# Kernel tuning notes

Measured on AMD Instinct MI355X. Metric: run time of the kernel, lower is better.

Reference implementation:

```python
import jax, jax.numpy as jnp
import numpy as np

# node types: 0=atac_region 1=gene 2=tad 3=protein 4=protein_name 5=enhancer
N = [25000, 15000, 4000, 12000, 12000, 15000]
FEAT = [257, 129, 128, 128, 129, 128]
# 19 relations of the HeteroConv, as (src_type, dst_type)
REL = [(2,0),(0,2),(2,1),(1,2),(0,1),(1,0),(3,3),(3,1),(1,3),(3,1),(1,3),(3,4),(4,3),(5,0),(0,5),(5,1),(1,5),(0,1),(1,0)]
E = 100000
H, HID = 128, 256
NAMES = ['atac','gene','tad','protein','pname','enh']


def setup_inputs():
    rng = np.random.default_rng(0)
    w = lambda *s: jnp.asarray((rng.standard_normal(s) / np.sqrt(s[-2])).astype(np.float32))
    z = lambda *s: jnp.zeros(s, dtype=jnp.float32)
    inp = {}
    for L in (0, 1):
        for t, nm in enumerate(NAMES):
            inp[f"x_{nm}{L}"] = jnp.asarray(rng.standard_normal((N[t], FEAT[t])).astype(np.float32))
            # sorted unique global node ids (x_map)
            inp[f"map_{nm}{L}"] = jnp.asarray(np.sort(rng.choice(2 * N[t], size=N[t], replace=False)).astype(np.int32))
        e = np.empty((len(REL), 2, E), dtype=np.int32)
        for r, (s, d) in enumerate(REL):
            e[r, 0] = rng.integers(0, N[s], E)
            e[r, 1] = rng.integers(0, N[d], E)
        inp[f"edges{L}"] = jnp.asarray(e)
    inp.update(W_in_atac=w(257, H), b_in_atac=z(H), W_in_gene=w(129, H), b_in_gene=z(H), W_in_pname=w(129, H), b_in_pname=z(H))
    inp.update(conv_wl=w(19, H, H), conv_bl=z(19, H), conv_wr=w(19, H, H))
    inp.update(mlp_w1=w(6, H, HID), mlp_b1=z(6, HID), mlp_w2=w(6, HID, H), mlp_b2=z(6, H))
    inp.update(gd_w1=w(H, HID), gd_b1=z(HID), gd_w2=w(HID, 1), gd_b2=z(1),
               gv_w1=w(H, HID), gv_b1=z(HID), gv_w2=w(HID, 1), gv_b2=z(1))
    return inp


def _sage(x_src, x_dst, eidx, wl, bl, wr):
    # PyG SAGEConv: out = lin_l(mean_{j in N(i)} x_src[j]) + lin_r(x_dst[i])
    src, dst = eidx[0], eidx[1]
    nd = x_dst.shape[0]
    agg = jax.ops.segment_sum(x_src[src], dst, num_segments=nd)
    cnt = jax.ops.segment_sum(jnp.ones((src.shape[0],), x_src.dtype), dst, num_segments=nd)
    mean = agg / jnp.maximum(cnt, 1.0)[:, None]
    return mean @ wl + bl + x_dst @ wr


def _hetero(xs, edges, wl, bl, wr):
    # HeteroConv with default sum aggregation across relations sharing a dst type
    out = {}
    for r, (s, d) in enumerate(REL):
        o = _sage(xs[s], xs[d], edges[r], wl[r], bl[r], wr[r])
        out[d] = out[d] + o if d in out else o
    return out


def _forward(fl, maps0, maps1, edges0, edges1):
    (x_atac0, x_gene0, x_tad0, x_protein0, x_pname0, x_enh0,
     x_atac1, x_gene1, x_tad1, x_protein1, x_pname1, x_enh1,
     W_in_atac, b_in_atac, W_in_gene, b_in_gene, W_in_pname, b_in_pname,
     conv_wl, conv_bl, conv_wr,
     mlp_w1, mlp_b1, mlp_w2, mlp_b2,
     gd_w1, gd_b1, gd_w2, gd_b2, gv_w1, gv_b1, gv_w2, gv_b2) = fl
    # input_linear applied to protein_name / atac_region / gene of every layer snapshot
    xs0 = [x_atac0 @ W_in_atac + b_in_atac, x_gene0 @ W_in_gene + b_in_gene, x_tad0,
           x_protein0, x_pname0 @ W_in_pname + b_in_pname, x_enh0]
    xs1 = [x_atac1 @ W_in_atac + b_in_atac, x_gene1 @ W_in_gene + b_in_gene, x_tad1,
           x_protein1, x_pname1 @ W_in_pname + b_in_pname, x_enh1]
    # layer 0 hetero conv + per-node-type layer MLP
    new0 = _hetero(xs0, edges0, conv_wl, conv_bl, conv_wr)
    new0 = {d: jax.nn.relu(x @ mlp_w1[d] + mlp_b1[d]) @ mlp_w2[d] + mlp_b2[d] for d, x in new0.items()}
    # mask-based cross-layer scatter: next_layer.x[dst_mask] = new_x[src_mask]
    # (x_maps sorted & unique -> equivalent gather via argmax of the O(N^2) equality mask)
    for d, x in new0.items():
        Mm = maps0[d][:, None] == maps1[d][None, :]   # [N0_d, N1_d] bool
        dst_mask = Mm.any(axis=0)                      # next-layer nodes present in layer 0
        pos = jnp.argmax(Mm, axis=0)                   # matching layer-0 row per next node
        xs1[d] = jnp.where(dst_mask[:, None], x[pos], xs1[d])
    # final layer: hetero conv only (no layer MLP, per encode())
    new1 = _hetero(xs1, edges1, conv_wl, conv_bl, conv_wr)
    g = new1[1]  # target = 'gene'
    p_drop = jax.nn.sigmoid(jax.nn.relu(g @ gd_w1 + gd_b1) @ gd_w2 + gd_b2)
    values = jax.nn.relu(g @ gv_w1 + gv_b1) @ gv_w2 + gv_b2
    return jnp.concatenate([p_drop, values], axis=-1)  # [N_gene, 2]


def reference(x_atac0, x_gene0, x_tad0, x_protein0, x_pname0, x_enh0,
              x_atac1, x_gene1, x_tad1, x_protein1, x_pname1, x_enh1,
              map_atac0, map_gene0, map_tad0, map_protein0, map_pname0, map_enh0,
              map_atac1, map_gene1, map_tad1, map_protein1, map_pname1, map_enh1,
              edges0, edges1,
              W_in_atac, b_in_atac, W_in_gene, b_in_gene, W_in_pname, b_in_pname,
              conv_wl, conv_bl, conv_wr,
              mlp_w1, mlp_b1, mlp_w2, mlp_b2,
              gd_w1, gd_b1, gd_w2, gd_b2, gv_w1, gv_b1, gv_w2, gv_b2):
    maps0 = [map_atac0, map_gene0, map_tad0, map_protein0, map_pname0, map_enh0]
    maps1 = [map_atac1, map_gene1, map_tad1, map_protein1, map_pname1, map_enh1]
    fl = (x_atac0, x_gene0, x_tad0, x_protein0, x_pname0, x_enh0,
          x_atac1, x_gene1, x_tad1, x_protein1, x_pname1, x_enh1,
          W_in_atac, b_in_atac, W_in_gene, b_in_gene, W_in_pname, b_in_pname,
          conv_wl, conv_bl, conv_wr,
          mlp_w1, mlp_b1, mlp_w2, mlp_b2,
          gd_w1, gd_b1, gd_w2, gd_b2, gv_w1, gv_b1, gv_w2, gv_b2)
    return _forward(fl, maps0, maps1, edges0, edges1)
```

## Files before the change

kernel.cpp:

```cpp
#include <hip/hip_runtime.h>
#include <math.h>

#define E_EDGES 100000

typedef unsigned short u16;
typedef unsigned int u32;

using bfrag = __attribute__((ext_vector_type(8))) short;
using ffrag = __attribute__((ext_vector_type(4))) float;

__device__ inline float bf2f(u32 u) { union { u32 i; float f; } c; c.i = u << 16; return c.f; }
__device__ inline u16 f2bf(float f) {
  union { u32 i; float f; } c; c.f = f;
  u32 u = c.i;
  return (u16)((u + 0x7FFFu + ((u >> 16) & 1u)) >> 16);
}

struct CsrArgs { int relid[24]; int lay[24]; int nd[24]; int rpoff[24];
                 int bkoff[24]; int bboff[24]; int nb[24]; };

struct AggAllArgs {
  const u16* xsrc[23];
  const int* rowptr[23];
  const int* esrc[23];
  u16* dst[23];
  int nd[23]; int pitch[23]; int koff[23]; int selfs[23];
};

struct WTStackArgs {
  int srcrel[23]; int grp[23]; long outoff[23]; int koff[23]; int pitch[23];
  int gnr[5]; int grel[5][6];
};

struct WTArgs { const float* W[15]; u16* out[15]; int K[15]; int N[15]; int Kpad[15]; };
struct PadArgs { const float* src[11]; u16* dst[11]; int K[11]; int Kpad8[11];
                 int total[11]; int aligned[11]; };
struct InLinBArgs { const u16* A[5]; const u16* WT[5]; const float* bias[5]; u16* C[5];
                    int M[5]; int Kpad[5]; };
struct BGemmArgs { const u16* A[5]; const u16* WT[5]; const float* bias[5]; u16* C[5];
                   const int* POS[5]; int M[5]; };
struct PosArgs { const int* m0[5]; const int* m1[5]; int* pos[5]; int n[5]; };
struct HeadArgs { const u16* WT[2]; const float* b1[2]; float* hid[2]; const float* A; int M; };
struct HeadRArgs { const float* hid[2]; const float* w2[2]; const float* b2[2]; float* out; int M; };

template <int AF32, int OF32, int RELU>
__global__ __launch_bounds__(256) void tgemm(const void* __restrict__ Av,
                                             const u16* __restrict__ WT,
                                             const float* __restrict__ bias,
                                             void* __restrict__ Cv,
                                             int M, int K, int Kpad, int N)
{
  __shared__ u16 sA[64 * 40];
  __shared__ u16 sB[128 * 40];
  const int tid = threadIdx.x;
  const int w = tid >> 6, lane = tid & 63;
  const int quad = lane >> 4, m = lane & 15;
  const int rowbase = blockIdx.x * 64;
  const int colbase = blockIdx.y * 128;
  const int sr = tid >> 2, sc = tid & 3;
  const int br = tid >> 1, bh = tid & 1;
  ffrag acc[8];
  #pragma unroll
  for (int i = 0; i < 8; i++) { acc[i][0] = 0.f; acc[i][1] = 0.f; acc[i][2] = 0.f; acc[i][3] = 0.f; }

  for (int kt = 0; kt < Kpad / 32; kt++) {
    int gr = rowbase + sr, gk = kt * 32 + sc * 8;
    uint4 st = make_uint4(0, 0, 0, 0);
    if (AF32) {
      const float* A = (const float*)Av;
      if (gr < M) {
        const float* row = A + (long)gr * K + gk;
        float v[8];
        #pragma unroll
        for (int i = 0; i < 8; i++) v[i] = (gk + i < K) ? row[i] : 0.f;
        st.x = (u32)f2bf(v[0]) | ((u32)f2bf(v[1]) << 16);
        st.y = (u32)f2bf(v[2]) | ((u32)f2bf(v[3]) << 16);
        st.z = (u32)f2bf(v[4]) | ((u32)f2bf(v[5]) << 16);
        st.w = (u32)f2bf(v[6]) | ((u32)f2bf(v[7]) << 16);
      }
    } else {
      const u16* A = (const u16*)Av;
      if (gr < M) st = *(const uint4*)(A + (long)gr * K + gk);
    }
    const u16* wrow = WT + (long)(colbase + br) * Kpad + kt * 32 + bh * 16;
    uint4 b0 = *(const uint4*)wrow;
    uint4 b1 = *(const uint4*)(wrow + 8);

    if (kt) __syncthreads();
    *(uint4*)&sA[sr * 40 + sc * 8] = st;
    *(uint4*)&sB[br * 40 + bh * 16] = b0;
    *(uint4*)&sB[br * 40 + bh * 16 + 8] = b1;
    __syncthreads();

    bfrag a = *(const bfrag*)&sA[(w * 16 + m) * 40 + quad * 8];
    #pragma unroll
    for (int ct = 0; ct < 8; ct++) {
      bfrag b = *(const bfrag*)&sB[(ct * 16 + m) * 40 + quad * 8];
      acc[ct] = __builtin_amdgcn_mfma_f32_16x16x32_bf16(a, b, acc[ct], 0, 0, 0);
    }
  }

  #pragma unroll
  for (int ct = 0; ct < 8; ct++) {
    int col = colbase + ct * 16 + m;
    float bv = bias ? bias[col] : 0.f;
    #pragma unroll
    for (int r = 0; r < 4; r++) {
      int row = rowbase + w * 16 + quad * 4 + r;
      if (row < M) {
        float v = acc[ct][r] + bv;
        if (RELU) v = fmaxf(v, 0.f);
        long off = (long)row * N + col;
        if (OF32) ((float*)Cv)[off] = v;
        else ((u16*)Cv)[off] = f2bf(v);
      }
    }
  }
}

__global__ __launch_bounds__(256) void tgemm_inb(InLinBArgs a)
{
  const int z = blockIdx.z;
  const int M = a.M[z], Kpad = a.Kpad[z];
  const int rowbase = blockIdx.x * 64;
  if (rowbase >= M) return;
  __shared__ u16 sA[64 * 40];
  __shared__ u16 sB[128 * 40];
  const int tid = threadIdx.x;
  const int w = tid >> 6, lane = tid & 63;
  const int quad = lane >> 4, m = lane & 15;
  const int sr = tid >> 2, sc = tid & 3;
  const int br = tid >> 1, bh = tid & 1;
  const u16* A = a.A[z];
  const u16* WT = a.WT[z];
  ffrag acc[8];
  #pragma unroll
  for (int i = 0; i < 8; i++) { acc[i][0] = 0.f; acc[i][1] = 0.f; acc[i][2] = 0.f; acc[i][3] = 0.f; }

  for (int kt = 0; kt < Kpad / 32; kt++) {
    int gr = rowbase + sr, gk = kt * 32 + sc * 8;
    uint4 st = make_uint4(0, 0, 0, 0);
    if (gr < M) st = *(const uint4*)(A + (long)gr * Kpad + gk);
    const u16* wrow = WT + (long)br * Kpad + kt * 32 + bh * 16;
    uint4 b0 = *(const uint4*)wrow;
    uint4 b1 = *(const uint4*)(wrow + 8);

    if (kt) __syncthreads();
    *(uint4*)&sA[sr * 40 + sc * 8] = st;
    *(uint4*)&sB[br * 40 + bh * 16] = b0;
    *(uint4*)&sB[br * 40 + bh * 16 + 8] = b1;
    __syncthreads();

    bfrag av = *(const bfrag*)&sA[(w * 16 + m) * 40 + quad * 8];
    #pragma unroll
    for (int ct = 0; ct < 8; ct++) {
      bfrag bv = *(const bfrag*)&sB[(ct * 16 + m) * 40 + quad * 8];
      acc[ct] = __builtin_amdgcn_mfma_f32_16x16x32_bf16(av, bv, acc[ct], 0, 0, 0);
    }
  }

  const float* bias = a.bias[z];
  u16* C = a.C[z];
  #pragma unroll
  for (int ct = 0; ct < 8; ct++) {
    int col = ct * 16 + m;
    float bv = bias[col];
    #pragma unroll
    for (int r = 0; r < 4; r++) {
      int row = rowbase + w * 16 + quad * 4 + r;
      if (row < M) C[(long)row * 128 + col] = f2bf(acc[ct][r] + bv);
    }
  }
}

__global__ __launch_bounds__(256) void tgemm_m1b(BGemmArgs a)
{
  const int z = blockIdx.z;
  const int M = a.M[z];
  const int rowbase = blockIdx.x * 64;
  if (rowbase >= M) return;
  const int colbase = blockIdx.y * 128;
  __shared__ u16 sA[64 * 40];
  __shared__ u16 sB[128 * 40];
  const int tid = threadIdx.x;
  const int w = tid >> 6, lane = tid & 63;
  const int quad = lane >> 4, m = lane & 15;
  const int sr = tid >> 2, sc = tid & 3;
  const int br = tid >> 1, bh = tid & 1;
  const u16* A = a.A[z];
  const u16* WT = a.WT[z];
  ffrag acc[8];
  #pragma unroll
  for (int i = 0; i < 8; i++) { acc[i][0] = 0.f; acc[i][1] = 0.f; acc[i][2] = 0.f; acc[i][3] = 0.f; }

  for (int kt = 0; kt < 4; kt++) {
    int gr = rowbase + sr, gk = kt * 32 + sc * 8;
    uint4 st = make_uint4(0, 0, 0, 0);
    if (gr < M) st = *(const uint4*)(A + (long)gr * 128 + gk);
    const u16* wrow = WT + (long)(colbase + br) * 128 + kt * 32 + bh * 16;
    uint4 b0 = *(const uint4*)wrow;
    uint4 b1 = *(const uint4*)(wrow + 8);

    if (kt) __syncthreads();
    *(uint4*)&sA[sr * 40 + sc * 8] = st;
    *(uint4*)&sB[br * 40 + bh * 16] = b0;
    *(uint4*)&sB[br * 40 + bh * 16 + 8] = b1;
    __syncthreads();

    bfrag av = *(const bfrag*)&sA[(w * 16 + m) * 40 + quad * 8];
    #pragma unroll
    for (int ct = 0; ct < 8; ct++) {
      bfrag bv = *(const bfrag*)&sB[(ct * 16 + m) * 40 + quad * 8];
      acc[ct] = __builtin_amdgcn_mfma_f32_16x16x32_bf16(av, bv, acc[ct], 0, 0, 0);
    }
  }

  const float* bias = a.bias[z];
  u16* C = a.C[z];
  #pragma unroll
  for (int ct = 0; ct < 8; ct++) {
    int col = colbase + ct * 16 + m;
    float bv = bias[col];
    #pragma unroll
    for (int r = 0; r < 4; r++) {
      int row = rowbase + w * 16 + quad * 4 + r;
      if (row < M) C[(long)row * 256 + col] = f2bf(fmaxf(acc[ct][r] + bv, 0.f));
    }
  }
}

__global__ __launch_bounds__(256) void tgemm_scatb(BGemmArgs a)
{
  const int z = blockIdx.z;
  const int M = a.M[z];
  const int rowbase = blockIdx.x * 64;
  if (rowbase >= M) return;
  __shared__ u16 sA[64 * 40];
  __shared__ u16 sB[128 * 40];
  const int tid = threadIdx.x;
  const int w = tid >> 6, lane = tid & 63;
  const int quad = lane >> 4, m = lane & 15;
  const int sr = tid >> 2, sc = tid & 3;
  const int br = tid >> 1, bh = tid & 1;
  const u16* A = a.A[z];
  const u16* WT = a.WT[z];
  ffrag acc[8];
  #pragma unroll
  for (int i = 0; i < 8; i++) { acc[i][0] = 0.f; acc[i][1] = 0.f; acc[i][2] = 0.f; acc[i][3] = 0.f; }

  for (int kt = 0; kt < 8; kt++) {
    int gr = rowbase + sr, gk = kt * 32 + sc * 8;
    uint4 st = make_uint4(0, 0, 0, 0);
    if (gr < M) st = *(const uint4*)(A + (long)gr * 256 + gk);
    const u16* wrow = WT + (long)br * 256 + kt * 32 + bh * 16;
    uint4 b0 = *(const uint4*)wrow;
    uint4 b1 = *(const uint4*)(wrow + 8);

    if (kt) __syncthreads();
    *(uint4*)&sA[sr * 40 + sc * 8] = st;
    *(uint4*)&sB[br * 40 + bh * 16] = b0;
    *(uint4*)&sB[br * 40 + bh * 16 + 8] = b1;
    __syncthreads();

    bfrag av = *(const bfrag*)&sA[(w * 16 + m) * 40 + quad * 8];
    #pragma unroll
    for (int ct = 0; ct < 8; ct++) {
      bfrag bv = *(const bfrag*)&sB[(ct * 16 + m) * 40 + quad * 8];
      acc[ct] = __builtin_amdgcn_mfma_f32_16x16x32_bf16(av, bv, acc[ct], 0, 0, 0);
    }
  }

  const int* POS = a.POS[z];
  const float* bias = a.bias[z];
  u16* C = a.C[z];
  #pragma unroll
  for (int ct = 0; ct < 8; ct++) {
    int col = ct * 16 + m;
    float bv = bias[col];
    #pragma unroll
    for (int r = 0; r < 4; r++) {
      int row = rowbase + w * 16 + quad * 4 + r;
      if (row < M) {
        int j = POS[row];
        if (j >= 0) C[(long)j * 128 + col] = f2bf(acc[ct][r] + bv);
      }
    }
  }
}

__global__ __launch_bounds__(256) void padcvt_kernel(PadArgs a)
{
  const int z = blockIdx.y;
  int idx = blockIdx.x * 256 + threadIdx.x;
  if (idx >= a.total[z]) return;
  const int kp8 = a.Kpad8[z];
  const int K = a.K[z];
  int row = idx / kp8;
  int c8 = idx - row * kp8;
  int base = c8 * 8;
  u32 wv[4];
  if (a.aligned[z]) {
    const float4* src = (const float4*)(a.src[z] + (long)row * K + base);
    float4 f0 = src[0];
    float4 f1 = src[1];
    wv[0] = (u32)f2bf(f0.x) | ((u32)f2bf(f0.y) << 16);
    wv[1] = (u32)f2bf(f0.z) | ((u32)f2bf(f0.w) << 16);
    wv[2] = (u32)f2bf(f1.x) | ((u32)f2bf(f1.y) << 16);
    wv[3] = (u32)f2bf(f1.z) | ((u32)f2bf(f1.w) << 16);
  } else {
    const float* src = a.src[z] + (long)row * K + base;
    #pragma unroll
    for (int i = 0; i < 4; i++) {
      float lo = (base + 2 * i     < K) ? src[2 * i]     : 0.f;
      float hi = (base + 2 * i + 1 < K) ? src[2 * i + 1] : 0.f;
      wv[i] = (u32)f2bf(lo) | ((u32)f2bf(hi) << 16);
    }
  }
  *(uint4*)(a.dst[z] + (long)row * (kp8 * 8) + base) = make_uint4(wv[0], wv[1], wv[2], wv[3]);
}

__global__ __launch_bounds__(256) void tgemm_head(HeadArgs a)
{
  const int z = blockIdx.z;
  const int M = a.M;
  const int rowbase = blockIdx.x * 64;
  const int colbase = blockIdx.y * 128;
  __shared__ u16 sA[64 * 40];
  __shared__ u16 sB[128 * 40];
  const int tid = threadIdx.x;
  const int w = tid >> 6, lane = tid & 63;
  const int quad = lane >> 4, m = lane & 15;
  const int sr = tid >> 2, sc = tid & 3;
  const int br = tid >> 1, bh = tid & 1;
  const float* A = a.A;
  const u16* WT = a.WT[z];
  ffrag acc[8];
  #pragma unroll
  for (int i = 0; i < 8; i++) { acc[i][0] = 0.f; acc[i][1] = 0.f; acc[i][2] = 0.f; acc[i][3] = 0.f; }

  for (int kt = 0; kt < 4; kt++) {
    int gr = rowbase + sr, gk = kt * 32 + sc * 8;
    uint4 st = make_uint4(0, 0, 0, 0);
    if (gr < M) {
      const float4* row = (const float4*)(A + (long)gr * 128 + gk);
      float4 f0 = row[0];
      float4 f1 = row[1];
      st.x = (u32)f2bf(f0.x) | ((u32)f2bf(f0.y) << 16);
      st.y = (u32)f2bf(f0.z) | ((u32)f2bf(f0.w) << 16);
      st.z = (u32)f2bf(f1.x) | ((u32)f2bf(f1.y) << 16);
      st.w = (u32)f2bf(f1.z) | ((u32)f2bf(f1.w) << 16);
    }
    const u16* wrow = WT + (long)(colbase + br) * 128 + kt * 32 + bh * 16;
    uint4 b0 = *(const uint4*)wrow;
    uint4 b1 = *(const uint4*)(wrow + 8);

    if (kt) __syncthreads();
    *(uint4*)&sA[sr * 40 + sc * 8] = st;
    *(uint4*)&sB[br * 40 + bh * 16] = b0;
    *(uint4*)&sB[br * 40 + bh * 16 + 8] = b1;
    __syncthreads();

    bfrag av = *(const bfrag*)&sA[(w * 16 + m) * 40 + quad * 8];
    #pragma unroll
    for (int ct = 0; ct < 8; ct++) {
      bfrag bv = *(const bfrag*)&sB[(ct * 16 + m) * 40 + quad * 8];
      acc[ct] = __builtin_amdgcn_mfma_f32_16x16x32_bf16(av, bv, acc[ct], 0, 0, 0);
    }
  }

  const float* bias = a.b1[z];
  float* C = a.hid[z];
  #pragma unroll
  for (int ct = 0; ct < 8; ct++) {
    int col = colbase + ct * 16 + m;
    float bv = bias[col];
    #pragma unroll
    for (int r = 0; r < 4; r++) {
      int row = rowbase + w * 16 + quad * 4 + r;
      if (row < M) C[(long)row * 256 + col] = fmaxf(acc[ct][r] + bv, 0.f);
    }
  }
}

__global__ __launch_bounds__(256) void bhist_kernel(const int* __restrict__ e0,
                                                    const int* __restrict__ e1,
                                                    int* __restrict__ bcnt, CsrArgs a)
{
  const int slot = blockIdx.x / 25;
  const int ch = blockIdx.x % 25;
  const int base = ch * 4096;
  const int n = (E_EDGES - base < 4096) ? (E_EDGES - base) : 4096;
  const int* E = a.lay[slot] ? e1 : e0;
  const int r = a.relid[slot];
  const int tid = threadIdx.x;
  __shared__ int h[256];
  h[tid] = 0;
  __syncthreads();
  const int* darr = E + (r * 2 + 1) * E_EDGES + base;
  for (int i = tid; i < n; i += 256) atomicAdd(&h[darr[i] >> 7], 1);
  __syncthreads();
  if (tid < a.nb[slot] && h[tid]) atomicAdd(&bcnt[a.bkoff[slot] + tid], h[tid]);
}

__global__ __launch_bounds__(256) void bscan_kernel(const int* __restrict__ bcnt,
// ... 130 lines not shown
  int sr = a.srcrel[slot];
  float v;
  if (sr >= 0) {
    v = wl[(long)sr * 16384 + krel * 128 + n];
  } else {
    int g = a.grp[slot];
    v = 0.f;
    for (int i = 0; i < a.gnr[g]; i++) v += wr[(long)a.grel[g][i] * 16384 + krel * 128 + n];
    if (t < 128) {
      float b = 0.f;
      for (int i = 0; i < a.gnr[g]; i++) b += bl[a.grel[g][i] * 128 + t];
      BLS[g * 128 + t] = b;
    }
  }
  WTG[a.outoff[slot] + (long)n * a.pitch[slot] + a.koff[slot] + krel] = f2bf(v);
}

__global__ __launch_bounds__(256) void wt_kernel(WTArgs a)
{
  int s = blockIdx.y;
  int idx = blockIdx.x * 256 + threadIdx.x;
  int K = a.K[s], N = a.N[s], Kpad = a.Kpad[s];
  if (idx >= N * Kpad) return;
  int n = idx / Kpad, k = idx - n * Kpad;
  a.out[s][idx] = (k < K) ? f2bf(a.W[s][(long)k * N + n]) : (u16)0;
}

__global__ __launch_bounds__(256) void pos_kernel(PosArgs a)
{
  int g = blockIdx.y;
  int i = blockIdx.x * 256 + threadIdx.x;
  if (i >= a.n[g]) return;
  int key = a.m0[g][i];
  const int* m1 = a.m1[g];
  int lo = 0, hi = a.n[g] - 1, pos = -1;
  while (lo <= hi) {
    int mid = (lo + hi) >> 1;
    int v = m1[mid];
    if (v == key) { pos = mid; break; }
    if (v < key) lo = mid + 1; else hi = mid - 1;
  }
  a.pos[g][i] = pos;
}

__global__ __launch_bounds__(256) void agg_all(AggAllArgs a)
{
  int slot = blockIdx.y;
  int grp = threadIdx.x >> 4;
  int lane = threadIdx.x & 15;
  int row = blockIdx.x * 16 + grp;
  if (row >= a.nd[slot]) return;
  u16* dst = a.dst[slot] + (long)row * a.pitch[slot] + a.koff[slot] + lane * 8;
  const uint4* x4 = (const uint4*)a.xsrc[slot];
  if (a.selfs[slot]) {
    *(uint4*)dst = x4[(long)row * 16 + lane];
    return;
  }
  const int* rp = a.rowptr[slot];
  int c0 = rp[row], c1 = rp[row + 1];
  const int* es = a.esrc[slot];
  float acc[8];
  #pragma unroll
  for (int i = 0; i < 8; i++) acc[i] = 0.f;
  int e = c0;
  for (; e + 4 <= c1; e += 4) {
    int s0 = es[e], s1 = es[e + 1], s2 = es[e + 2], s3 = es[e + 3];
    uint4 v0 = x4[(long)s0 * 16 + lane];
    uint4 v1 = x4[(long)s1 * 16 + lane];
    uint4 v2 = x4[(long)s2 * 16 + lane];
    uint4 v3 = x4[(long)s3 * 16 + lane];
    const u32* w0 = (const u32*)&v0;
    const u32* w1 = (const u32*)&v1;
    const u32* w2 = (const u32*)&v2;
    const u32* w3 = (const u32*)&v3;
    #pragma unroll
    for (int i = 0; i < 4; i++) {
      acc[2*i]   += bf2f(w0[i] & 0xFFFF) + bf2f(w1[i] & 0xFFFF)
                  + bf2f(w2[i] & 0xFFFF) + bf2f(w3[i] & 0xFFFF);
      acc[2*i+1] += bf2f(w0[i] >> 16) + bf2f(w1[i] >> 16)
                  + bf2f(w2[i] >> 16) + bf2f(w3[i] >> 16);
    }
  }
  for (; e < c1; e++) {
    uint4 v = x4[(long)es[e] * 16 + lane];
    const u32* wv = (const u32*)&v;
    #pragma unroll
    for (int i = 0; i < 4; i++) {
      acc[2*i]   += bf2f(wv[i] & 0xFFFF);
      acc[2*i+1] += bf2f(wv[i] >> 16);
    }
  }
  int c = c1 - c0;
  float inv = 1.f / (float)(c > 1 ? c : 1);
  u32 o[4];
  #pragma unroll
  for (int i = 0; i < 4; i++)
    o[i] = (u32)f2bf(acc[2*i] * inv) | ((u32)f2bf(acc[2*i+1] * inv) << 16);
  *(uint4*)dst = make_uint4(o[0], o[1], o[2], o[3]);
}

__global__ __launch_bounds__(256) void head_reduce2(HeadRArgs a)
{
  int wave = threadIdx.x >> 6, lane = threadIdx.x & 63;
  int row = blockIdx.x * 4 + wave;
  int z = blockIdx.y;
  if (row >= a.M) return;
  const float* h = a.hid[z] + (long)row * 256;
  const float* w2 = a.w2[z];
  float s = h[lane] * w2[lane] + h[lane + 64] * w2[lane + 64]
          + h[lane + 128] * w2[lane + 128] + h[lane + 192] * w2[lane + 192];
  #pragma unroll
  for (int off = 32; off >= 1; off >>= 1) s += __shfl_down(s, off, 64);
  if (lane == 0) {
    float v = s + a.b2[z][0];
    if (z == 0) v = 1.0f / (1.0f + expf(-v));
    a.out[row * 2 + z] = v;
  }
}

extern "C" void kernel_launch(void* const* d_in, const int* in_sizes, int n_in,
                              void* d_out, int out_size, void* d_ws, size_t ws_size,
                              hipStream_t stream)
{
  static const int NT[6] = {25000, 15000, 4000, 12000, 12000, 15000};
  static const int REL_S[19] = {2,0,2,1,0,1,3,3,1,3,1,3,4,5,0,5,1,0,1};
  static const int REL_D[19] = {0,2,1,2,1,0,3,1,3,1,3,4,3,0,5,1,5,1,0};

  auto xin   = [&](int t, int L) { return (const float*)d_in[L * 13 + 2 * t]; };
  auto mapin = [&](int t, int L) { return (const int*)d_in[L * 13 + 2 * t + 1]; };
  const int* edges0 = (const int*)d_in[12];
  const int* edges1 = (const int*)d_in[25];
  const float* W_in_atac  = (const float*)d_in[26];
  const float* b_in_atac  = (const float*)d_in[27];
  const float* W_in_gene  = (const float*)d_in[28];
  const float* b_in_gene  = (const float*)d_in[29];
  const float* W_in_pname = (const float*)d_in[30];
  const float* b_in_pname = (const float*)d_in[31];
  const float* conv_wl = (const float*)d_in[32];
  const float* conv_bl = (const float*)d_in[33];
  const float* conv_wr = (const float*)d_in[34];
  const float* mlp_w1 = (const float*)d_in[35];
  const float* mlp_b1 = (const float*)d_in[36];
  const float* mlp_w2 = (const float*)d_in[37];
  const float* mlp_b2 = (const float*)d_in[38];
  const float* gd_w1 = (const float*)d_in[39];
  const float* gd_b1 = (const float*)d_in[40];
  const float* gd_w2 = (const float*)d_in[41];
  const float* gd_b2 = (const float*)d_in[42];
  const float* gv_w1 = (const float*)d_in[43];
  const float* gv_b1 = (const float*)d_in[44];
  const float* gv_w2 = (const float*)d_in[45];
  const float* gv_b2 = (const float*)d_in[46];
  float* out = (float*)d_out;

  static const int GD[5]       = {0, 1, 2, 3, 5};
  static const int GNR[5]      = {4, 6, 2, 4, 2};
  static const int GRELS[5][6] = {{0,5,13,18,0,0},{2,4,7,9,15,17},{1,3,0,0,0,0},
                                  {6,8,10,12,0,0},{14,16,0,0,0,0}};
  static const int GPITCH[5]   = {640, 896, 384, 640, 384};

  float* fp = (float*)d_ws;
  auto takef = [&](size_t n) { float* q = fp; fp += n; return q; };
  float* BLS  = takef(5 * 128);
  float* G1   = takef((size_t)15000 * 128);
  u16* bp = (u16*)fp;
  auto takeb = [&](size_t n) { u16* q = bp; bp += n; return q; };
  u16* XB0[6]; u16* XB1[6];
  XB0[0] = takeb((size_t)25000 * 128);
  XB0[1] = takeb((size_t)15000 * 128);
  XB0[2] = takeb((size_t)4000 * 128);
  XB0[3] = takeb((size_t)12000 * 128);
  XB0[4] = takeb((size_t)12000 * 128);
  XB0[5] = takeb((size_t)15000 * 128);
  XB1[0] = takeb((size_t)25000 * 128);
  XB1[1] = takeb((size_t)15000 * 128);
  XB1[2] = takeb((size_t)4000 * 128);
  XB1[3] = takeb((size_t)12000 * 128);
  XB1[4] = nullptr;
  XB1[5] = takeb((size_t)15000 * 128);
  u16* ABUF = takeb((size_t)44416000);
  u16* ABUFg[5];
  {
    long o = 0;
    for (int g = 0; g < 5; g++) { ABUFg[g] = ABUF + o; o += (long)NT[GD[g]] * GPITCH[g]; }
  }
  u16* NWB  = takeb((size_t)71000 * 128);
  u16* HIDB = takeb((size_t)71000 * 256);
  u16* NWBg[5]; u16* HIDBg[5];
  {
    long o = 0;
    for (int g = 0; g < 5; g++) { NWBg[g] = NWB + o * 128; HIDBg[g] = HIDB + o * 256; o += NT[GD[g]]; }
  }
  u16* WTG  = takeb(376832);
  u16* WTIA = takeb(128 * 288);
  u16* WTIG = takeb(128 * 160);
  u16* WTIP = takeb(128 * 160);
  u16* WTM1 = takeb((size_t)5 * 32768);
  u16* WTM2 = takeb((size_t)5 * 32768);
  u16* WTHD = takeb(32768);
  u16* WTHV = takeb(32768);
  uintptr_t ipa = ((uintptr_t)bp + 15) & ~(uintptr_t)15;
  int* ip = (int*)ipa;
  auto takei = [&](size_t n) { int* q = ip; ip += n; return q; };
  int* RP    = takei(366024);
  int* BCNT  = takei(4704);
  int* BBASE = takei(4728);
  int* BCUR  = takei(4704);
  int* POSB  = takei(71000);
  int* ESRC  = takei((size_t)24 * E_EDGES);
  u32* TMP = (u32*)ABUF;
  float* HIDF0 = (float*)ABUF;
  float* HIDF1 = (float*)(ABUF + (size_t)15000 * 256 * 2);
  u16* PAD[5];
  PAD[0] = ABUF;
  PAD[1] = ABUF +  7200000;
  PAD[2] = ABUF +  9600000;
  PAD[3] = ABUF + 11520000;
  PAD[4] = ABUF + 18720000;

  long gbaseT[5];
  {
    long o = 0;
    for (int g = 0; g < 5; g++) { gbaseT[g] = o; o += (long)128 * GPITCH[g]; }
  }
  int* POSg[5];
  {
    int o = 0;
    for (int g = 0; g < 5; g++) { POSg[g] = POSB + o; o += NT[GD[g]]; }
  }

  {
    WTStackArgs wa{};
    int j = 0;
    for (int g = 0; g < 5; g++) {
      wa.gnr[g] = GNR[g];
      for (int i = 0; i < 6; i++) wa.grel[g][i] = GRELS[g][i];
      for (int s = 0; s <= GNR[g]; s++, j++) {
        wa.srcrel[j] = (s < GNR[g]) ? GRELS[g][s] : -1;
        wa.grp[j] = g;
        wa.outoff[j] = gbaseT[g];
        wa.koff[j] = s * 128;
        wa.pitch[j] = GPITCH[g];
      }
    }
    hipLaunchKernelGGL(wtstack_kernel, dim3(64, 23), dim3(256), 0, stream,
// ... 50 lines not shown
    auto add = [&](int s, const u16* A, const u16* WT, const float* b, u16* C,
                   int M, int Kpad) {
      ia.A[s] = A; ia.WT[s] = WT; ia.bias[s] = b; ia.C[s] = C;
      ia.M[s] = M; ia.Kpad[s] = Kpad;
    };
    add(0, PAD[0], WTIA, b_in_atac,  XB0[0], 25000, 288);
    add(1, PAD[1], WTIG, b_in_gene,  XB0[1], 15000, 160);
    add(2, PAD[2], WTIP, b_in_pname, XB0[4], 12000, 160);
    add(3, PAD[3], WTIA, b_in_atac,  XB1[0], 25000, 288);
    add(4, PAD[4], WTIG, b_in_gene,  XB1[1], 15000, 160);
    hipLaunchKernelGGL(tgemm_inb, dim3(391, 1, 5), dim3(256), 0, stream, ia);
  }

  static const int L0R[18] = {0,1,2,3,4,5,6,7,8,9,10,12,13,14,15,16,17,18};
  static const int L1R[6]  = {2, 4, 7, 9, 15, 17};
  int rpoffByRel[19], slotByRel[19], rpoff1[19], slot1[19];
  CsrArgs cc{};
  {
    int ro = 0, bo = 0, s = 0;
    for (int i = 0; i < 18; i++, s++) {
      int r = L0R[i];
      cc.relid[s] = r; cc.lay[s] = 0; int nd = NT[REL_D[r]];
      cc.nd[s] = nd; cc.rpoff[s] = ro;
      cc.bkoff[s] = bo; cc.bboff[s] = bo + s; cc.nb[s] = (nd + 127) >> 7;
      rpoffByRel[r] = ro; slotByRel[r] = s;
      ro += nd + 1; bo += cc.nb[s];
    }
    for (int i = 0; i < 6; i++, s++) {
      int r = L1R[i];
      cc.relid[s] = r; cc.lay[s] = 1;
      cc.nd[s] = 15000; cc.rpoff[s] = ro;
      cc.bkoff[s] = bo; cc.bboff[s] = bo + s; cc.nb[s] = (15000 + 127) >> 7;
      rpoff1[r] = ro; slot1[r] = s;
      ro += 15001; bo += cc.nb[s];
    }
    hipMemsetAsync(BCNT, 0, (size_t)bo * 4, stream);
    hipLaunchKernelGGL(bhist_kernel, dim3(24 * 25), dim3(256), 0, stream, edges0, edges1, BCNT, cc);
    hipLaunchKernelGGL(bscan_kernel, dim3(24), dim3(256), 0, stream, BCNT, BBASE, BCUR, cc);
    hipLaunchKernelGGL(bucket_scatter, dim3(24 * 25), dim3(256), 0, stream,
                       edges0, edges1, BCUR, TMP, cc);
    hipLaunchKernelGGL(bucket_to_csr, dim3(196, 24), dim3(256), 0, stream, TMP, BBASE, RP, ESRC, cc);
  }

  {
    AggAllArgs aa{};
    int j = 0;
    for (int g = 0; g < 5; g++) {
      int d = GD[g];
      for (int i = 0; i < GNR[g]; i++, j++) {
        int r = GRELS[g][i];
        aa.xsrc[j]   = XB0[REL_S[r]];
        aa.rowptr[j] = RP + rpoffByRel[r];
        aa.esrc[j]   = ESRC + (long)slotByRel[r] * E_EDGES;
        aa.dst[j] = ABUFg[g]; aa.nd[j] = NT[d]; aa.pitch[j] = GPITCH[g];
        aa.koff[j] = i * 128; aa.selfs[j] = 0;
      }
      aa.xsrc[j] = XB0[d]; aa.rowptr[j] = nullptr; aa.esrc[j] = nullptr;
      aa.dst[j] = ABUFg[g]; aa.nd[j] = NT[d]; aa.pitch[j] = GPITCH[g];
      aa.koff[j] = GNR[g] * 128; aa.selfs[j] = 1; j++;
    }
    hipLaunchKernelGGL(agg_all, dim3(1563, 23), dim3(256), 0, stream, aa);
  }
  {
    InLinBArgs ia{};
    for (int g = 0; g < 5; g++) {
      ia.A[g] = ABUFg[g]; ia.WT[g] = WTG + gbaseT[g]; ia.bias[g] = BLS + g * 128;
      ia.C[g] = NWBg[g]; ia.M[g] = NT[GD[g]]; ia.Kpad[g] = GPITCH[g];
    }
    hipLaunchKernelGGL(tgemm_inb, dim3(391, 1, 5), dim3(256), 0, stream, ia);
  }
  {
    BGemmArgs ba{};
    for (int g = 0; g < 5; g++) {
      int d = GD[g];
      ba.A[g] = NWBg[g]; ba.WT[g] = WTM1 + (long)g * 32768; ba.bias[g] = mlp_b1 + d * 256;
      ba.C[g] = HIDBg[g]; ba.POS[g] = nullptr; ba.M[g] = NT[d];
    }
    hipLaunchKernelGGL(tgemm_m1b, dim3(391, 2, 5), dim3(256), 0, stream, ba);
  }
  {
    BGemmArgs ba{};
    for (int g = 0; g < 5; g++) {
      int d = GD[g];
      ba.A[g] = HIDBg[g]; ba.WT[g] = WTM2 + (long)g * 32768; ba.bias[g] = mlp_b2 + d * 128;
      ba.C[g] = XB1[d]; ba.POS[g] = POSg[g]; ba.M[g] = NT[d];
    }
    hipLaunchKernelGGL(tgemm_scatb, dim3(391, 1, 5), dim3(256), 0, stream, ba);
  }

  {
    AggAllArgs aa{};
    for (int i = 0; i < 6; i++) {
      int r = L1R[i];
      aa.xsrc[i]   = XB1[REL_S[r]];
      aa.rowptr[i] = RP + rpoff1[r];
      aa.esrc[i]   = ESRC + (long)slot1[r] * E_EDGES;
      aa.dst[i] = ABUF; aa.nd[i] = 15000; aa.pitch[i] = 896;
      aa.koff[i] = i * 128; aa.selfs[i] = 0;
    }
    aa.xsrc[6] = XB1[1]; aa.rowptr[6] = nullptr; aa.esrc[6] = nullptr;
    aa.dst[6] = ABUF; aa.nd[6] = 15000; aa.pitch[6] = 896;
    aa.koff[6] = 6 * 128; aa.selfs[6] = 1;
    hipLaunchKernelGGL(agg_all, dim3(938, 7), dim3(256), 0, stream, aa);
    hipLaunchKernelGGL(HIP_KERNEL_NAME(tgemm<0,1,0>), dim3(235, 1), dim3(256), 0, stream,
                       (const void*)ABUF, WTG + gbaseT[1], BLS + 1 * 128, (void*)G1,
                       15000, 896, 896, 128);
  }

  {
    HeadArgs ha{};
    ha.WT[0] = WTHD; ha.WT[1] = WTHV;
    ha.b1[0] = gd_b1; ha.b1[1] = gv_b1;
    ha.hid[0] = HIDF0; ha.hid[1] = HIDF1;
    ha.A = G1; ha.M = 15000;
    hipLaunchKernelGGL(tgemm_head, dim3(235, 2, 2), dim3(256), 0, stream, ha);
    HeadRArgs hr{};
    hr.hid[0] = HIDF0; hr.hid[1] = HIDF1;
    hr.w2[0] = gd_w2; hr.w2[1] = gv_w2;
    hr.b2[0] = gd_b2; hr.b2[1] = gv_b2;
    hr.out = out; hr.M = 15000;
    hipLaunchKernelGGL(head_reduce2, dim3(3750, 2), dim3(256), 0, stream, hr);
  }
}
```

Baseline: 547.2 us.

## Fuse conv linear and two-layer MLP into one kernel, drop self-copy slots

Layer-0 conv projection, MLP hidden layer and MLP output with position scatter now run in one fused kernel that keeps the intermediate 64-row tiles in LDS instead of writing them to global buffers between three launches. The aggregation kernel no longer copies self features into the concatenated buffer; the GEMMs read self features straight from the node feature array by splitting the K range. The layer-1 conv output is stored as bf16 rather than fp32, and the head kernel reads it without converting. In exchange, the larger LDS footprint (about 50KB) lowers occupancy, and the fused kernel serializes its three GEMM phases within each block.

```diff
diff --git a/kernel.cpp b/kernel.cpp
--- a/kernel.cpp
+++ b/kernel.cpp
@@ -20,11 +20,11 @@
                  int bkoff[24]; int bboff[24]; int nb[24]; };
 
 struct AggAllArgs {
-  const u16* xsrc[23];
-  const int* rowptr[23];
-  const int* esrc[23];
-  u16* dst[23];
-  int nd[23]; int pitch[23]; int koff[23]; int selfs[23];
+  const u16* xsrc[18];
+  const int* rowptr[18];
+  const int* esrc[18];
+  u16* dst[18];
+  int nd[18]; int pitch[18]; int koff[18];
 };
 
 struct WTStackArgs {
@@ -37,86 +37,14 @@
                  int total[11]; int aligned[11]; };
 struct InLinBArgs { const u16* A[5]; const u16* WT[5]; const float* bias[5]; u16* C[5];
                     int M[5]; int Kpad[5]; };
-struct BGemmArgs { const u16* A[5]; const u16* WT[5]; const float* bias[5]; u16* C[5];
-                   const int* POS[5]; int M[5]; };
+struct FusedArgs {
+  const u16* A[5]; const u16* selfA[5]; const u16* WTC[5]; const float* biasC[5];
+  const u16* W1[5]; const float* b1[5]; const u16* W2[5]; const float* b2[5];
+  const int* POS[5]; u16* C[5]; int M[5]; int kself[5]; int Kpad[5];
+};
 struct PosArgs { const int* m0[5]; const int* m1[5]; int* pos[5]; int n[5]; };
-struct HeadArgs { const u16* WT[2]; const float* b1[2]; float* hid[2]; const float* A; int M; };
+struct HeadArgs { const u16* WT[2]; const float* b1[2]; float* hid[2]; const u16* A; int M; };
 struct HeadRArgs { const float* hid[2]; const float* w2[2]; const float* b2[2]; float* out; int M; };
-
-template <int AF32, int OF32, int RELU>
-__global__ __launch_bounds__(256) void tgemm(const void* __restrict__ Av,
-                                             const u16* __restrict__ WT,
-                                             const float* __restrict__ bias,
-                                             void* __restrict__ Cv,
-                                             int M, int K, int Kpad, int N)
-{
-  __shared__ u16 sA[64 * 40];
-  __shared__ u16 sB[128 * 40];
-  const int tid = threadIdx.x;
-  const int w = tid >> 6, lane = tid & 63;
-  const int quad = lane >> 4, m = lane & 15;
-  const int rowbase = blockIdx.x * 64;
-  const int colbase = blockIdx.y * 128;
-  const int sr = tid >> 2, sc = tid & 3;
-  const int br = tid >> 1, bh = tid & 1;
-  ffrag acc[8];
-  #pragma unroll
-  for (int i = 0; i < 8; i++) { acc[i][0] = 0.f; acc[i][1] = 0.f; acc[i][2] = 0.f; acc[i][3] = 0.f; }
-
-  for (int kt = 0; kt < Kpad / 32; kt++) {
-    int gr = rowbase + sr, gk = kt * 32 + sc * 8;
-    uint4 st = make_uint4(0, 0, 0, 0);
-    if (AF32) {
-      const float* A = (const float*)Av;
-      if (gr < M) {
-        const float* row = A + (long)gr * K + gk;
-        float v[8];
-        #pragma unroll
-        for (int i = 0; i < 8; i++) v[i] = (gk + i < K) ? row[i] : 0.f;
-        st.x = (u32)f2bf(v[0]) | ((u32)f2bf(v[1]) << 16);
-        st.y = (u32)f2bf(v[2]) | ((u32)f2bf(v[3]) << 16);
-        st.z = (u32)f2bf(v[4]) | ((u32)f2bf(v[5]) << 16);
-        st.w = (u32)f2bf(v[6]) | ((u32)f2bf(v[7]) << 16);
-      }
-    } else {
-      const u16* A = (const u16*)Av;
-      if (gr < M) st = *(const uint4*)(A + (long)gr * K + gk);
-    }
-    const u16* wrow = WT + (long)(colbase + br) * Kpad + kt * 32 + bh * 16;
-    uint4 b0 = *(const uint4*)wrow;
-    uint4 b1 = *(const uint4*)(wrow + 8);
-
-    if (kt) __syncthreads();
-    *(uint4*)&sA[sr * 40 + sc * 8] = st;
-    *(uint4*)&sB[br * 40 + bh * 16] = b0;
-    *(uint4*)&sB[br * 40 + bh * 16 + 8] = b1;
-    __syncthreads();
-
-    bfrag a = *(const bfrag*)&sA[(w * 16 + m) * 40 + quad * 8];
-    #pragma unroll
-    for (int ct = 0; ct < 8; ct++) {
-      bfrag b = *(const bfrag*)&sB[(ct * 16 + m) * 40 + quad * 8];
-      acc[ct] = __builtin_amdgcn_mfma_f32_16x16x32_bf16(a, b, acc[ct], 0, 0, 0);
-    }
-  }
-
-  #pragma unroll
-  for (int ct = 0; ct < 8; ct++) {
-    int col = colbase + ct * 16 + m;
-    float bv = bias ? bias[col] : 0.f;
-    #pragma unroll
-    for (int r = 0; r < 4; r++) {
-      int row = rowbase + w * 16 + quad * 4 + r;
-      if (row < M) {
-        float v = acc[ct][r] + bv;
-        if (RELU) v = fmaxf(v, 0.f);
-        long off = (long)row * N + col;
-        if (OF32) ((float*)Cv)[off] = v;
-        else ((u16*)Cv)[off] = f2bf(v);
-      }
-    }
-  }
-}
 
 __global__ __launch_bounds__(256) void tgemm_inb(InLinBArgs a)
 {
@@ -173,66 +101,154 @@
   }
 }
 
-__global__ __launch_bounds__(256) void tgemm_m1b(BGemmArgs a)
+__global__ __launch_bounds__(256) void fused_mlp(FusedArgs a)
 {
   const int z = blockIdx.z;
   const int M = a.M[z];
   const int rowbase = blockIdx.x * 64;
   if (rowbase >= M) return;
-  const int colbase = blockIdx.y * 128;
-  __shared__ u16 sA[64 * 40];
-  __shared__ u16 sB[128 * 40];
+  __shared__ u16 LDS[25088];
+  u16* sB  = LDS;
+  u16* sA  = LDS + 5120;
+  u16* m1  = LDS + 7680;
+  u16* m2b = LDS + 5120;
+  u16* m2a = LDS + 16384;
   const int tid = threadIdx.x;
   const int w = tid >> 6, lane = tid & 63;
   const int quad = lane >> 4, m = lane & 15;
   const int sr = tid >> 2, sc = tid & 3;
   const int br = tid >> 1, bh = tid & 1;
+  const int kself = a.kself[z], Kpad = a.Kpad[z];
   const u16* A = a.A[z];
-  const u16* WT = a.WT[z];
-  ffrag acc[8];
-  #pragma unroll
-  for (int i = 0; i < 8; i++) { acc[i][0] = 0.f; acc[i][1] = 0.f; acc[i][2] = 0.f; acc[i][3] = 0.f; }
-
-  for (int kt = 0; kt < 4; kt++) {
-    int gr = rowbase + sr, gk = kt * 32 + sc * 8;
-    uint4 st = make_uint4(0, 0, 0, 0);
-    if (gr < M) st = *(const uint4*)(A + (long)gr * 128 + gk);
-    const u16* wrow = WT + (long)(colbase + br) * 128 + kt * 32 + bh * 16;
-    uint4 b0 = *(const uint4*)wrow;
-    uint4 b1 = *(const uint4*)(wrow + 8);
-
-    if (kt) __syncthreads();
-    *(uint4*)&sA[sr * 40 + sc * 8] = st;
-    *(uint4*)&sB[br * 40 + bh * 16] = b0;
-    *(uint4*)&sB[br * 40 + bh * 16 + 8] = b1;
-    __syncthreads();
-
-    bfrag av = *(const bfrag*)&sA[(w * 16 + m) * 40 + quad * 8];
+  const u16* selfA = a.selfA[z];
+
+  {
+    const u16* WT = a.WTC[z];
+    ffrag acc[8];
+    #pragma unroll
+    for (int i = 0; i < 8; i++) { acc[i][0] = 0.f; acc[i][1] = 0.f; acc[i][2] = 0.f; acc[i][3] = 0.f; }
+    for (int kt = 0; kt < Kpad / 32; kt++) {
+      int gr = rowbase + sr, gk = kt * 32 + sc * 8;
+      uint4 st = make_uint4(0, 0, 0, 0);
+      if (gr < M) {
+        const u16* src = (gk < kself) ? (A + (long)gr * kself + gk)
+                                      : (selfA + (long)gr * 128 + (gk - kself));
+        st = *(const uint4*)src;
+      }
+      const u16* wrow = WT + (long)br * Kpad + kt * 32 + bh * 16;
+      uint4 b0 = *(const uint4*)wrow;
+      uint4 b1 = *(const uint4*)(wrow + 8);
+
+      if (kt) __syncthreads();
+      *(uint4*)&sA[sr * 40 + sc * 8] = st;
+      *(uint4*)&sB[br * 40 + bh * 16] = b0;
+      *(uint4*)&sB[br * 40 + bh * 16 + 8] = b1;
+      __syncthreads();
+
+      bfrag av = *(const bfrag*)&sA[(w * 16 + m) * 40 + quad * 8];
+      #pragma unroll
+      for (int ct = 0; ct < 8; ct++) {
+        bfrag bv = *(const bfrag*)&sB[(ct * 16 + m) * 40 + quad * 8];
+        acc[ct] = __builtin_amdgcn_mfma_f32_16x16x32_bf16(av, bv, acc[ct], 0, 0, 0);
+      }
+    }
+    const float* bc = a.biasC[z];
     #pragma unroll
     for (int ct = 0; ct < 8; ct++) {
-      bfrag bv = *(const bfrag*)&sB[(ct * 16 + m) * 40 + quad * 8];
-      acc[ct] = __builtin_amdgcn_mfma_f32_16x16x32_bf16(av, bv, acc[ct], 0, 0, 0);
-    }
-  }
-
-  const float* bias = a.bias[z];
-  u16* C = a.C[z];
-  #pragma unroll
-  for (int ct = 0; ct < 8; ct++) {
-    int col = colbase + ct * 16 + m;
-    float bv = bias[col];
-    #pragma unroll
-    for (int r = 0; r < 4; r++) {
-      int row = rowbase + w * 16 + quad * 4 + r;
-      if (row < M) C[(long)row * 256 + col] = f2bf(fmaxf(acc[ct][r] + bv, 0.f));
-    }
-  }
-}
-
-__global__ __launch_bounds__(256) void tgemm_scatb(BGemmArgs a)
-{
-  const int z = blockIdx.z;
-  const int M = a.M[z];
+      int col = ct * 16 + m;
+      float bv = bc[col];
+      #pragma unroll
+      for (int r = 0; r < 4; r++) {
+        int row = w * 16 + quad * 4 + r;
+        m1[row * 136 + col] = f2bf(acc[ct][r] + bv);
+      }
+    }
+  }
+
+  {
+    const u16* W1 = a.W1[z];
+    const float* b1p = a.b1[z];
+    for (int h = 0; h < 2; h++) {
+      ffrag acch[8];
+      #pragma unroll
+      for (int i = 0; i < 8; i++) { acch[i][0] = 0.f; acch[i][1] = 0.f; acch[i][2] = 0.f; acch[i][3] = 0.f; }
+      for (int kt = 0; kt < 4; kt++) {
+        const u16* wrow = W1 + (long)(h * 128 + br) * 128 + kt * 32 + bh * 16;
+        uint4 b0 = *(const uint4*)wrow;
+        uint4 b1v = *(const uint4*)(wrow + 8);
+        __syncthreads();
+        *(uint4*)&sB[br * 40 + bh * 16] = b0;
+        *(uint4*)&sB[br * 40 + bh * 16 + 8] = b1v;
+        __syncthreads();
+        bfrag av = *(const bfrag*)&m1[(w * 16 + m) * 136 + kt * 32 + quad * 8];
+        #pragma unroll
+        for (int ct = 0; ct < 8; ct++) {
+          bfrag bv = *(const bfrag*)&sB[(ct * 16 + m) * 40 + quad * 8];
+          acch[ct] = __builtin_amdgcn_mfma_f32_16x16x32_bf16(av, bv, acch[ct], 0, 0, 0);
+        }
+      }
+      u16* dstm = h ? m2b : m2a;
+      if (h) __syncthreads();
+      #pragma unroll
+      for (int ct = 0; ct < 8; ct++) {
+        int col = ct * 16 + m;
+        float bv = b1p[h * 128 + col];
+        #pragma unroll
+        for (int r = 0; r < 4; r++) {
+          int row = w * 16 + quad * 4 + r;
+          dstm[row * 136 + col] = f2bf(fmaxf(acch[ct][r] + bv, 0.f));
+        }
+      }
+    }
+  }
+
+  {
+    const u16* W2 = a.W2[z];
+    ffrag acc2[8];
+    #pragma unroll
+    for (int i = 0; i < 8; i++) { acc2[i][0] = 0.f; acc2[i][1] = 0.f; acc2[i][2] = 0.f; acc2[i][3] = 0.f; }
+    for (int kt = 0; kt < 8; kt++) {
+      const u16* wrow = W2 + (long)br * 256 + kt * 32 + bh * 16;
+      uint4 b0 = *(const uint4*)wrow;
+      uint4 b1v = *(const uint4*)(wrow + 8);
+      __syncthreads();
+      *(uint4*)&sB[br * 40 + bh * 16] = b0;
+      *(uint4*)&sB[br * 40 + bh * 16 + 8] = b1v;
+      __syncthreads();
+      const u16* msrc = (kt < 4) ? m2a : m2b;
+      bfrag av = *(const bfrag*)&msrc[(w * 16 + m) * 136 + (kt & 3) * 32 + quad * 8];
+      #pragma unroll
+      for (int ct = 0; ct < 8; ct++) {
+        bfrag bv = *(const bfrag*)&sB[(ct * 16 + m) * 40 + quad * 8];
+        acc2[ct] = __builtin_amdgcn_mfma_f32_16x16x32_bf16(av, bv, acc2[ct], 0, 0, 0);
+      }
+    }
+    const int* POS = a.POS[z];
+    const float* b2p = a.b2[z];
+    u16* C = a.C[z];
+    #pragma unroll
+    for (int ct = 0; ct < 8; ct++) {
+      int col = ct * 16 + m;
+      float bv = b2p[col];
+      #pragma unroll
+      for (int r = 0; r < 4; r++) {
+        int row = rowbase + w * 16 + quad * 4 + r;
+        if (row < M) {
+          int j = POS[row];
+          if (j >= 0) C[(long)j * 128 + col] = f2bf(acc2[ct][r] + bv);
+        }
+      }
+    }
+  }
+}
+
+__global__ __launch_bounds__(256) void conv_l1(const u16* __restrict__ A,
+                                               const u16* __restrict__ selfA,
+                                               const u16* __restrict__ WT,
+                                               const float* __restrict__ bias,
+                                               u16* __restrict__ C,
+                                               int M, int kself, int Kpad)
+{
   const int rowbase = blockIdx.x * 64;
   if (rowbase >= M) return;
   __shared__ u16 sA[64 * 40];
@@ -242,17 +258,19 @@
   const int quad = lane >> 4, m = lane & 15;
   const int sr = tid >> 2, sc = tid & 3;
   const int br = tid >> 1, bh = tid & 1;
-  const u16* A = a.A[z];
-  const u16* WT = a.WT[z];
   ffrag acc[8];
   #pragma unroll
   for (int i = 0; i < 8; i++) { acc[i][0] = 0.f; acc[i][1] = 0.f; acc[i][2] = 0.f; acc[i][3] = 0.f; }
 
-  for (int kt = 0; kt < 8; kt++) {
+  for (int kt = 0; kt < Kpad / 32; kt++) {
     int gr = rowbase + sr, gk = kt * 32 + sc * 8;
     uint4 st = make_uint4(0, 0, 0, 0);
-    if (gr < M) st = *(const uint4*)(A + (long)gr * 256 + gk);
-    const u16* wrow = WT + (long)br * 256 + kt * 32 + bh * 16;
+    if (gr < M) {
+      const u16* src = (gk < kself) ? (A + (long)gr * kself + gk)
+                                    : (selfA + (long)gr * 128 + (gk - kself));
+      st = *(const uint4*)src;
+    }
+    const u16* wrow = WT + (long)br * Kpad + kt * 32 + bh * 16;
     uint4 b0 = *(const uint4*)wrow;
     uint4 b1 = *(const uint4*)(wrow + 8);
 
@@ -270,9 +288,6 @@
     }
   }
 
-  const int* POS = a.POS[z];
-  const float* bias = a.bias[z];
-  u16* C = a.C[z];
   #pragma unroll
   for (int ct = 0; ct < 8; ct++) {
     int col = ct * 16 + m;
@@ -280,10 +295,7 @@
     #pragma unroll
     for (int r = 0; r < 4; r++) {
       int row = rowbase + w * 16 + quad * 4 + r;
-      if (row < M) {
-        int j = POS[row];
-        if (j >= 0) C[(long)j * 128 + col] = f2bf(acc[ct][r] + bv);
-      }
+      if (row < M) C[(long)row * 128 + col] = f2bf(acc[ct][r] + bv);
     }
   }
 }
@@ -332,7 +344,7 @@
   const int quad = lane >> 4, m = lane & 15;
   const int sr = tid >> 2, sc = tid & 3;
   const int br = tid >> 1, bh = tid & 1;
-  const float* A = a.A;
+  const u16* A = a.A;
   const u16* WT = a.WT[z];
   ffrag acc[8];
   #pragma unroll
@@ -341,15 +353,7 @@
   for (int kt = 0; kt < 4; kt++) {
     int gr = rowbase + sr, gk = kt * 32 + sc * 8;
     uint4 st = make_uint4(0, 0, 0, 0);
-    if (gr < M) {
-      const float4* row = (const float4*)(A + (long)gr * 128 + gk);
-      float4 f0 = row[0];
-      float4 f1 = row[1];
-      st.x = (u32)f2bf(f0.x) | ((u32)f2bf(f0.y) << 16);
-      st.y = (u32)f2bf(f0.z) | ((u32)f2bf(f0.w) << 16);
-      st.z = (u32)f2bf(f1.x) | ((u32)f2bf(f1.y) << 16);
-      st.w = (u32)f2bf(f1.z) | ((u32)f2bf(f1.w) << 16);
-    }
+    if (gr < M) st = *(const uint4*)(A + (long)gr * 128 + gk);
     const u16* wrow = WT + (long)(colbase + br) * 128 + kt * 32 + bh * 16;
     uint4 b0 = *(const uint4*)wrow;
     uint4 b1 = *(const uint4*)(wrow + 8);
@@ -586,10 +590,6 @@
   if (row >= a.nd[slot]) return;
   u16* dst = a.dst[slot] + (long)row * a.pitch[slot] + a.koff[slot] + lane * 8;
   const uint4* x4 = (const uint4*)a.xsrc[slot];
-  if (a.selfs[slot]) {
-    *(uint4*)dst = x4[(long)row * 16 + lane];
-    return;
-  }
   const int* rp = a.rowptr[slot];
   int c0 = rp[row], c1 = rp[row + 1];
   const int* es = a.esrc[slot];
@@ -692,11 +692,11 @@
   static const int GRELS[5][6] = {{0,5,13,18,0,0},{2,4,7,9,15,17},{1,3,0,0,0,0},
                                   {6,8,10,12,0,0},{14,16,0,0,0,0}};
   static const int GPITCH[5]   = {640, 896, 384, 640, 384};
+  static const int GPA[5]      = {512, 768, 256, 512, 256};
 
   float* fp = (float*)d_ws;
   auto takef = [&](size_t n) { float* q = fp; fp += n; return q; };
   float* BLS  = takef(5 * 128);
-  float* G1   = takef((size_t)15000 * 128);
   u16* bp = (u16*)fp;
   auto takeb = [&](size_t n) { u16* q = bp; bp += n; return q; };
   u16* XB0[6]; u16* XB1[6];
@@ -712,19 +712,13 @@
   XB1[3] = takeb((size_t)12000 * 128);
   XB1[4] = nullptr;
   XB1[5] = takeb((size_t)15000 * 128);
-  u16* ABUF = takeb((size_t)44416000);
+  u16* ABUF = takeb((size_t)35328000);
   u16* ABUFg[5];
   {
     long o = 0;
-    for (int g = 0; g < 5; g++) { ABUFg[g] = ABUF + o; o += (long)NT[GD[g]] * GPITCH[g]; }
-  }
-  u16* NWB  = takeb((size_t)71000 * 128);
-  u16* HIDB = takeb((size_t)71000 * 256);
-  u16* NWBg[5]; u16* HIDBg[5];
-  {
-    long o = 0;
-    for (int g = 0; g < 5; g++) { NWBg[g] = NWB + o * 128; HIDBg[g] = HIDB + o * 256; o += NT[GD[g]]; }
-  }
+    for (int g = 0; g < 5; g++) { ABUFg[g] = ABUF + o; o += (long)NT[GD[g]] * GPA[g]; }
+  }
+  u16* G1B  = takeb((size_t)15000 * 128);
   u16* WTG  = takeb(376832);
   u16* WTIA = takeb(128 * 288);
   u16* WTIG = takeb(128 * 160);
@@ -881,40 +875,24 @@
         aa.xsrc[j]   = XB0[REL_S[r]];
         aa.rowptr[j] = RP + rpoffByRel[r];
         aa.esrc[j]   = ESRC + (long)slotByRel[r] * E_EDGES;
-        aa.dst[j] = ABUFg[g]; aa.nd[j] = NT[d]; aa.pitch[j] = GPITCH[g];
-        aa.koff[j] = i * 128; aa.selfs[j] = 0;
+        aa.dst[j] = ABUFg[g]; aa.nd[j] = NT[d]; aa.pitch[j] = GPA[g];
+        aa.koff[j] = i * 128;
       }
-      aa.xsrc[j] = XB0[d]; aa.rowptr[j] = nullptr; aa.esrc[j] = nullptr;
-      aa.dst[j] = ABUFg[g]; aa.nd[j] = NT[d]; aa.pitch[j] = GPITCH[g];
-      aa.koff[j] = GNR[g] * 128; aa.selfs[j] = 1; j++;
-    }
-    hipLaunchKernelGGL(agg_all, dim3(1563, 23), dim3(256), 0, stream, aa);
-  }
-  {
-    InLinBArgs ia{};
-    for (int g = 0; g < 5; g++) {
-      ia.A[g] = ABUFg[g]; ia.WT[g] = WTG + gbaseT[g]; ia.bias[g] = BLS + g * 128;
-      ia.C[g] = NWBg[g]; ia.M[g] = NT[GD[g]]; ia.Kpad[g] = GPITCH[g];
-    }
-    hipLaunchKernelGGL(tgemm_inb, dim3(391, 1, 5), dim3(256), 0, stream, ia);
-  }
-  {
-    BGemmArgs ba{};
+    }
+    hipLaunchKernelGGL(agg_all, dim3(1563, 18), dim3(256), 0, stream, aa);
+  }
+  {
+    FusedArgs fa{};
     for (int g = 0; g < 5; g++) {
       int d = GD[g];
-      ba.A[g] = NWBg[g]; ba.WT[g] = WTM1 + (long)g * 32768; ba.bias[g] = mlp_b1 + d * 256;
-      ba.C[g] = HIDBg[g]; ba.POS[g] = nullptr; ba.M[g] = NT[d];
-    }
-    hipLaunchKernelGGL(tgemm_m1b, dim3(391, 2, 5), dim3(256), 0, stream, ba);
-  }
-  {
-    BGemmArgs ba{};
-    for (int g = 0; g < 5; g++) {
-      int d = GD[g];
-      ba.A[g] = HIDBg[g]; ba.WT[g] = WTM2 + (long)g * 32768; ba.bias[g] = mlp_b2 + d * 128;
-      ba.C[g] = XB1[d]; ba.POS[g] = POSg[g]; ba.M[g] = NT[d];
-    }
-    hipLaunchKernelGGL(tgemm_scatb, dim3(391, 1, 5), dim3(256), 0, stream, ba);
+      fa.A[g] = ABUFg[g]; fa.selfA[g] = XB0[d];
+      fa.WTC[g] = WTG + gbaseT[g]; fa.biasC[g] = BLS + g * 128;
+      fa.W1[g] = WTM1 + (long)g * 32768; fa.b1[g] = mlp_b1 + d * 256;
+      fa.W2[g] = WTM2 + (long)g * 32768; fa.b2[g] = mlp_b2 + d * 128;
+      fa.POS[g] = POSg[g]; fa.C[g] = XB1[d];
+      fa.M[g] = NT[d]; fa.kself[g] = GPA[g]; fa.Kpad[g] = GPITCH[g];
+    }
+    hipLaunchKernelGGL(fused_mlp, dim3(391, 1, 5), dim3(256), 0, stream, fa);
   }
 
   {
@@ -924,16 +902,13 @@
       aa.xsrc[i]   = XB1[REL_S[r]];
       aa.rowptr[i] = RP + rpoff1[r];
       aa.esrc[i]   = ESRC + (long)slot1[r] * E_EDGES;
-      aa.dst[i] = ABUF; aa.nd[i] = 15000; aa.pitch[i] = 896;
-      aa.koff[i] = i * 128; aa.selfs[i] = 0;
-    }
-    aa.xsrc[6] = XB1[1]; aa.rowptr[6] = nullptr; aa.esrc[6] = nullptr;
-    aa.dst[6] = ABUF; aa.nd[6] = 15000; aa.pitch[6] = 896;
-    aa.koff[6] = 6 * 128; aa.selfs[6] = 1;
-    hipLaunchKernelGGL(agg_all, dim3(938, 7), dim3(256), 0, stream, aa);
-    hipLaunchKernelGGL(HIP_KERNEL_NAME(tgemm<0,1,0>), dim3(235, 1), dim3(256), 0, stream,
-                       (const void*)ABUF, WTG + gbaseT[1], BLS + 1 * 128, (void*)G1,
-                       15000, 896, 896, 128);
+      aa.dst[i] = ABUF; aa.nd[i] = 15000; aa.pitch[i] = 768;
+      aa.koff[i] = i * 128;
+    }
+    hipLaunchKernelGGL(agg_all, dim3(938, 6), dim3(256), 0, stream, aa);
+    hipLaunchKernelGGL(conv_l1, dim3(235), dim3(256), 0, stream,
+                       ABUF, XB1[1], WTG + gbaseT[1], BLS + 1 * 128, G1B,
+                       15000, 768, 896);
   }
 
   {
@@ -941,7 +916,7 @@
     ha.WT[0] = WTHD; ha.WT[1] = WTHV;
     ha.b1[0] = gd_b1; ha.b1[1] = gv_b1;
     ha.hid[0] = HIDF0; ha.hid[1] = HIDF1;
-    ha.A = G1; ha.M = 15000;
+    ha.A = G1B; ha.M = 15000;
     hipLaunchKernelGGL(tgemm_head, dim3(235, 2, 2), dim3(256), 0, stream, ha);
     HeadRArgs hr{};
     hr.hid[0] = HIDF0; hr.hid[1] = HIDF1;
```

Measured after the change: 519.0 us. 1.05x faster.
